# Kernel tuning notes

Hardware: AMD Instinct MI355X
Metric: run time of the kernel (lower is better)

Reference implementation:

```python
import jax, jax.numpy as jnp
import numpy as np

NEG_SLOPE = 0.2  # PyG GATConv default leaky_relu slope

def gat_conv(x, src, dst, W, a_src, a_dst, bias, N):
    # Linear transform
    h = x @ W                      # [N, D]
    # Per-node attention logits (heads=1)
    al_src = h @ a_src             # [N]
    al_dst = h @ a_dst             # [N]
    e = jax.nn.leaky_relu(al_src[src] + al_dst[dst], NEG_SLOPE)  # [E]
    # Segment softmax over incoming edges of each destination node
    m = jax.ops.segment_max(e, dst, num_segments=N)
    ex = jnp.exp(e - m[dst])
    denom = jax.ops.segment_sum(ex, dst, num_segments=N)
    alpha = ex / denom[dst]        # [E]
    # Weighted scatter-aggregate of source features
    out = jax.ops.segment_sum(h[src] * alpha[:, None], dst, num_segments=N)
    return out + bias

def setup_inputs() -> dict:
    key = jax.random.key(0)
    ks = jax.random.split(key, 10)
    N, E, F_in, H, O = 50000, 800000, 128, 64, 64
    x = jax.random.normal(ks[0], (N, F_in), dtype=jnp.float32)
    edge_index = jax.random.randint(ks[1], (2, E), 0, N, dtype=jnp.int32)
    s = lambda k, shp, fan: jax.random.normal(k, shp, dtype=jnp.float32) / np.sqrt(fan)
    return {
        'x': x, 'edge_index': edge_index,
        'W1': s(ks[2], (F_in, H), F_in), 'a_src1': s(ks[3], (H,), H), 'a_dst1': s(ks[4], (H,), H), 'b1': jnp.zeros((H,), jnp.float32),
        'W2': s(ks[5], (H, O), H), 'a_src2': s(ks[6], (O,), O), 'a_dst2': s(ks[7], (O,), O), 'b2': jnp.zeros((O,), jnp.float32),
    }

def reference(x, edge_index, W1, a_src1, a_dst1, b1, W2, a_src2, a_dst2, b2):
    N = x.shape[0]
    loops = jnp.arange(N, dtype=edge_index.dtype)  # PyG adds self-loops by default
    src = jnp.concatenate([edge_index[0], loops])
    dst = jnp.concatenate([edge_index[1], loops])
    h = gat_conv(x, src, dst, W1, a_src1, a_dst1, b1, N)
    h = jax.nn.relu(h)
    # dropout(p=0.6) is identity in eval mode
    out = gat_conv(h, src, dst, W2, a_src2, a_dst2, b2, N)
    return out
```

## Files before the change

kernel.cpp:

```cpp
#include <hip/hip_runtime.h>
#include <hip/hip_bf16.h>

#define DEV static __device__ __forceinline__

typedef short bf16x8 __attribute__((ext_vector_type(8)));
typedef float f32x4  __attribute__((ext_vector_type(4)));
typedef unsigned u32x4 __attribute__((ext_vector_type(4)));

union U4 { uint4 u; bf16x8 s; };

DEV float b2f(__hip_bfloat16 v) { return __bfloat162float(v); }
DEV float lrelu(float e) { return e > 0.f ? e : 0.2f * e; }

DEV unsigned short f2bu(float f) {
    __hip_bfloat16 b = __float2bfloat16(f);
    return *reinterpret_cast<unsigned short*>(&b);
}
DEV float bu2f(unsigned short u) { return __uint_as_float((unsigned)u << 16); }

DEV float loadF(const void* p, size_t i, int f32) {
    if (f32) return ((const float*)p)[i];
    return b2f(((const __hip_bfloat16*)p)[i]);
}

DEV uint4 pack8(const unsigned short* t) {
    uint4 v;
    v.x = (unsigned)t[0] | ((unsigned)t[1] << 16);
    v.y = (unsigned)t[2] | ((unsigned)t[3] << 16);
    v.z = (unsigned)t[4] | ((unsigned)t[5] << 16);
    v.w = (unsigned)t[6] | ((unsigned)t[7] << 16);
    return v;
}

DEV u32x4 pack8v(const unsigned short* t) {
    u32x4 v;
    v.x = (unsigned)t[0] | ((unsigned)t[1] << 16);
    v.y = (unsigned)t[2] | ((unsigned)t[3] << 16);
    v.z = (unsigned)t[4] | ((unsigned)t[5] << 16);
    v.w = (unsigned)t[6] | ((unsigned)t[7] << 16);
    return v;
}

DEV void edge_sd(int i, int E, const int* __restrict__ src, const int* __restrict__ dst,
                 int& s, int& d) {
    if (i < E) { s = src[i]; d = dst[i]; }
    else       { s = d = i - E; }
}

DEV int detect_wave(const void* p, int n, int lane) {
    const unsigned short* u16 = (const unsigned short*)p;
    bool insane = false;
#pragma unroll
    for (int r = 0; r < 4; ++r) {
        int idx = lane + r * 64;
        if (idx < n) {
            unsigned short u = u16[idx];
            unsigned e = (u >> 7) & 0xFFu;
            insane |= (e >= 0xC8u) || (e == 0u && (u & 0x7Fu) != 0u);
        }
    }
    return (__ballot(insane) != 0ull) ? 1 : 0;
}

#define G_BIN 128

__global__ __launch_bounds__(256) void k_fused1(
    const void* __restrict__ x, const void* __restrict__ W,
    const void* __restrict__ a_s, const void* __restrict__ a_d,
    __hip_bfloat16* __restrict__ h, float* __restrict__ als, float* __restrict__ ald,
    int N, int gb, int nx, int nW1,
    const int* __restrict__ src, const int* __restrict__ dst,
    int* __restrict__ hist, int E, int EA, int chunk,
    const void* a5, int n5, const void* a6, int n6, const void* a7, int n7,
    const void* a8, int n8, const void* a9, int n9,
    int* __restrict__ flags)
{
    const int tid = threadIdx.x;
    const int bid = blockIdx.x;

    if (bid >= gb) {
        if (bid == gb + G_BIN) {
            const void* ps[9] = {x, W, a_s, a_d, a5, a6, a7, a8, a9};
            const int   ns[9] = {nx, nW1, 64, 64, n5, n6, n7, n8, n9};
            const int w = tid >> 6, lane = tid & 63;
            for (int k = w; k < 9; k += 4) {
                int f = detect_wave(ps[k], ns[k], lane);
                if (lane == 0) flags[k] = f;
            }
            return;
        }
        __shared__ int cnt[256];
        cnt[tid] = 0;
        __syncthreads();
        const int cb = bid - gb;
        const int lo = cb * chunk;
        const int hi = min(lo + chunk, EA);
        for (int i = lo + tid; i < hi; i += 256) {
            int s, d; edge_sd(i, E, src, dst, s, d);
            atomicAdd(&cnt[d >> 8], 1);
        }
        __syncthreads();
        hist[cb * 256 + tid] = cnt[tid];
        return;
    }

    __shared__ __align__(16) unsigned short sMem[2 * 64 * 136];
    __shared__ float sAs[64], sAd[64];
    __shared__ int sFl[4];
    unsigned short* sA = sMem;
    unsigned short* sB = sMem + 64 * 136;
    float* sOut = (float*)sMem;

    {
        const void* ps4[4] = {x, W, a_s, a_d};
        const int   ns4[4] = {nx, nW1, 64, 64};
        const int w = tid >> 6, lane = tid & 63;
        int f = detect_wave(ps4[w], ns4[w], lane);
        if (lane == 0) sFl[w] = f;
    }
    __syncthreads();
    const int fx = sFl[0], fw = sFl[1];

    const int row0 = bid * 64;
    if (tid < 64) sAs[tid] = loadF(a_s, tid, sFl[2]);
    else if (tid < 128) sAd[tid - 64] = loadF(a_d, tid - 64, sFl[3]);

    if (!fx) {
        const uint4* xg = (const uint4*)x;
#pragma unroll
        for (int it = 0; it < 2; ++it) {
            int g = tid + it * 256;
            int r = g >> 4, c16 = g & 15;
            uint4 v = (row0 + r < N) ? xg[(size_t)(row0 + r) * 16 + c16]
                                     : make_uint4(0, 0, 0, 0);
            *(uint4*)(sA + r * 136 + c16 * 8) = v;
        }
    } else {
        for (int i = tid; i < 64 * 128; i += 256) {
            int r = i >> 7, k = i & 127;
            float v = (row0 + r < N) ? ((const float*)x)[(size_t)(row0 + r) * 128 + k] : 0.f;
            sA[r * 136 + k] = f2bu(v);
        }
    }
    if (!fw) {
        const unsigned short* Wg = (const unsigned short*)W;
        const int n = tid & 63;
        int k0 = (tid >> 6) * 8;
#pragma unroll
        for (int rep = 0; rep < 4; ++rep, k0 += 32) {
            unsigned short t[8];
#pragma unroll
            for (int j = 0; j < 8; ++j) t[j] = Wg[(size_t)(k0 + j) * 64 + n];
            *(uint4*)(sB + n * 136 + k0) = pack8(t);
        }
    } else {
        const float* Wg = (const float*)W;
        for (int i = tid; i < 128 * 64; i += 256) {
            int k = i >> 6, n = i & 63;
            sB[n * 136 + k] = f2bu(Wg[i]);
        }
    }
    __syncthreads();

    const int w = tid >> 6, lane = tid & 63;
    const int m0 = w * 16;
    const int qr = lane >> 4;
    const int lc = lane & 15;

    bf16x8 afrag[4];
#pragma unroll
    for (int c = 0; c < 4; ++c) {
        U4 u; u.u = *(const uint4*)(sA + (m0 + lc) * 136 + c * 32 + qr * 8);
        afrag[c] = u.s;
    }
    f32x4 accs[4];
#pragma unroll
    for (int nt = 0; nt < 4; ++nt) {
        f32x4 acc = {0.f, 0.f, 0.f, 0.f};
#pragma unroll
        for (int c = 0; c < 4; ++c) {
            U4 u; u.u = *(const uint4*)(sB + (nt * 16 + lc) * 136 + c * 32 + qr * 8);
            acc = __builtin_amdgcn_mfma_f32_16x16x32_bf16(afrag[c], u.s, acc, 0, 0, 0);
        }
        accs[nt] = acc;
    }
    __syncthreads();

#pragma unroll
    for (int nt = 0; nt < 4; ++nt)
#pragma unroll
        for (int reg = 0; reg < 4; ++reg)
            sOut[(m0 + qr * 4 + reg) * 68 + nt * 16 + lc] = accs[nt][reg];
    __syncthreads();

    {
        const int r = tid >> 2, seg = tid & 3;
        const int row = row0 + r;
        const float* po = sOut + r * 68 + seg * 16;
        float ps = 0.f, pd = 0.f;
        unsigned short ob[16];
#pragma unroll
        for (int i = 0; i < 16; ++i) {
            float v = po[i];
            ps = fmaf(v, sAs[seg * 16 + i], ps);
            pd = fmaf(v, sAd[seg * 16 + i], pd);
            ob[i] = f2bu(v);
        }
        if (row < N) {
            uint4* hp = (uint4*)((unsigned short*)h + (size_t)row * 64 + seg * 16);
            hp[0] = pack8(ob);
            hp[1] = pack8(ob + 8);
        }
        ps += __shfl_xor(ps, 1, 64); ps += __shfl_xor(ps, 2, 64);
        pd += __shfl_xor(pd, 1, 64); pd += __shfl_xor(pd, 2, 64);
        if (seg == 0 && row < N) { als[row] = ps; ald[row] = pd; }
    }
}

__global__ __launch_bounds__(256) void k_binC2(
    const int* __restrict__ src, const int* __restrict__ dst,
    const int* __restrict__ hist, int* __restrict__ btot,
    unsigned* __restrict__ ebuf, int E, int EA, int chunk)
{
    __shared__ int sm[256];
    __shared__ int cur[256];
    const int tid = threadIdx.x;
    const int cb = blockIdx.x;

    int tot = 0, mine = 0;
#pragma unroll 4
    for (int c = 0; c < G_BIN; ++c) {
        int v = hist[c * 256 + tid];
        tot += v;
        if (c < cb) mine += v;
    }
    if (cb == 0) btot[tid] = tot;
    sm[tid] = tot;
    __syncthreads();
#pragma unroll
    for (int off = 1; off < 256; off <<= 1) {
        int t = (tid >= off) ? sm[tid - off] : 0;
        __syncthreads();
        sm[tid] += t;
        __syncthreads();
    }
    cur[tid] = (sm[tid] - tot) + mine;
    __syncthreads();
    const int lo = cb * chunk;
    const int hi = min(lo + chunk, EA);
    for (int i = lo + tid; i < hi; i += 256) {
        int s, d; edge_sd(i, E, src, dst, s, d);
        int pos = atomicAdd(&cur[d >> 8], 1);
        ebuf[pos] = ((unsigned)(d & 255) << 17) | (unsigned)s;
    }
}

__global__ __launch_bounds__(256) void k_binD(
    const unsigned* __restrict__ ebuf, const int* __restrict__ btot,
    int* __restrict__ row_ptr, int* __restrict__ col, int N)
{
    __shared__ int sm[256];
    __shared__ int cnt[256];
    __shared__ int pfx[256];
    const int tid = threadIdx.x;
    const int b = blockIdx.x;
    {
        int v = btot[tid];
        sm[tid] = v;
        __syncthreads();
#pragma unroll
        for (int off = 1; off < 256; off <<= 1) {
            int t = (tid >= off) ? sm[tid - off] : 0;
            __syncthreads();
            sm[tid] += t;
            __syncthreads();
        }
    }
    const int lo = (b == 0) ? 0 : sm[b - 1];
    const int hi = sm[b];
    cnt[tid] = 0;
    __syncthreads();
    for (int i = lo + tid; i < hi; i += 256)
        atomicAdd(&cnt[ebuf[i] >> 17], 1);
    __syncthreads();
    const int c = cnt[tid];
    pfx[tid] = c;
    __syncthreads();
#pragma unroll
    for (int off = 1; off < 256; off <<= 1) {
        int t = (tid >= off) ? pfx[tid - off] : 0;
        __syncthreads();
        pfx[tid] += t;
        __syncthreads();
    }
    const int excl = pfx[tid] - c;
    const int d = b * 256 + tid;
    if (d <= N) row_ptr[d] = lo + excl;
    __syncthreads();
    cnt[tid] = lo + excl;
    __syncthreads();
    for (int i = lo + tid; i < hi; i += 256) {
        unsigned v = ebuf[i];
        int pos = atomicAdd(&cnt[v >> 17], 1);
        col[pos] = (int)(v & 0x1FFFFu);
    }
}

__global__ __launch_bounds__(256) void k_gemm2(
    __hip_bfloat16* __restrict__ agg, const void* __restrict__ b1,
    const void* __restrict__ W, const void* __restrict__ a_s,
    const void* __restrict__ a_d, const int* __restrict__ flags,
    float* __restrict__ als, float* __restrict__ ald, int N)
{
    __shared__ __align__(16) unsigned short sMem[2 * 64 * 72];
    __shared__ float sAs[64], sAd[64], sBias[64];
    unsigned short* sA = sMem;
    unsigned short* sB = sMem + 64 * 72;
    float* sOut = (float*)sMem;

    const int tid = threadIdx.x;
    const int row0 = blockIdx.x * 64;
    const int fw = flags[5];

    if (tid < 64) sAs[tid] = loadF(a_s, tid, flags[6]);
    else if (tid < 128) sAd[tid - 64] = loadF(a_d, tid - 64, flags[7]);
    else if (tid < 192) sBias[tid - 128] = loadF(b1, tid - 128, flags[4]);
    __syncthreads();

    {
        const uint4* ag = (const uint4*)agg;
#pragma unroll
        for (int it = 0; it < 2; ++it) {
            int g = tid + it * 256;
            int r = g >> 3, c8 = g & 7;
            uint4 v = (row0 + r < N) ? ag[(size_t)(row0 + r) * 8 + c8]
                                     : make_uint4(0, 0, 0, 0);
            unsigned short in[8] = {
                (unsigned short)(v.x & 0xFFFF), (unsigned short)(v.x >> 16),
                (unsigned short)(v.y & 0xFFFF), (unsigned short)(v.y >> 16),
                (unsigned short)(v.z & 0xFFFF), (unsigned short)(v.z >> 16),
                (unsigned short)(v.w & 0xFFFF), (unsigned short)(v.w >> 16)};
            unsigned short ob[8];
#pragma unroll
            for (int j = 0; j < 8; ++j) {
                float t = bu2f(in[j]) + sBias[c8 * 8 + j];
                ob[j] = f2bu(t > 0.f ? t : 0.f);
            }
            *(uint4*)(sA + r * 72 + c8 * 8) = pack8(ob);
        }
    }
    if (!fw) {
        const unsigned short* Wg = (const unsigned short*)W;
        const int n = tid & 63;
        int k0 = (tid >> 6) * 8;
#pragma unroll
        for (int rep = 0; rep < 2; ++rep, k0 += 32) {
            unsigned short t[8];
#pragma unroll
            for (int j = 0; j < 8; ++j) t[j] = Wg[(size_t)(k0 + j) * 64 + n];
            *(uint4*)(sB + n * 72 + k0) = pack8(t);
        }
    } else {
        const float* Wg = (const float*)W;
        for (int i = tid; i < 64 * 64; i += 256) {
            int k = i >> 6, n = i & 63;
            sB[n * 72 + k] = f2bu(Wg[i]);
        }
    }
    __syncthreads();

    const int w = tid >> 6, lane = tid & 63;
    const int m0 = w * 16;
    const int qr = lane >> 4, lc = lane & 15;

    bf16x8 afrag[2];
#pragma unroll
    for (int c = 0; c < 2; ++c) {
        U4 u; u.u = *(const uint4*)(sA + (m0 + lc) * 72 + c * 32 + qr * 8);
        afrag[c] = u.s;
    }
    f32x4 accs[4];
#pragma unroll
    for (int nt = 0; nt < 4; ++nt) {
        f32x4 acc = {0.f, 0.f, 0.f, 0.f};
#pragma unroll
        for (int c = 0; c < 2; ++c) {
            U4 u; u.u = *(const uint4*)(sB + (nt * 16 + lc) * 72 + c * 32 + qr * 8);
            acc = __builtin_amdgcn_mfma_f32_16x16x32_bf16(afrag[c], u.s, acc, 0, 0, 0);
        }
        accs[nt] = acc;
    }
    __syncthreads();
#pragma unroll
    for (int nt = 0; nt < 4; ++nt)
#pragma unroll
        for (int reg = 0; reg < 4; ++reg)
            sOut[(m0 + qr * 4 + reg) * 68 + nt * 16 + lc] = accs[nt][reg];
    __syncthreads();

    {
        const int r = tid >> 2, seg = tid & 3;
        const int row = row0 + r;
        const float* po = sOut + r * 68 + seg * 16;
        float ps = 0.f, pd = 0.f;
        unsigned short ob[16];
#pragma unroll
        for (int i = 0; i < 16; ++i) {
            float v = po[i];
            ps = fmaf(v, sAs[seg * 16 + i], ps);
            pd = fmaf(v, sAd[seg * 16 + i], pd);
            ob[i] = f2bu(v);
        }
        if (row < N) {
            uint4* hp = (uint4*)((unsigned short*)agg + (size_t)row * 64 + seg * 16);
            hp[0] = pack8(ob);
            hp[1] = pack8(ob + 8);
        }
        ps += __shfl_xor(ps, 1, 64); ps += __shfl_xor(ps, 2, 64);
        pd += __shfl_xor(pd, 1, 64); pd += __shfl_xor(pd, 2, 64);
        if (seg == 0 && row < N) { als[row] = ps; ald[row] = pd; }
    }
}

__global__ __launch_bounds__(256) void k_gather(
    const int* __restrict__ row_ptr, const int* __restrict__ col,
    const float* __restrict__ als, const float* __restrict__ ald,
    const __hip_bfloat16* __restrict__ h,
    __hip_bfloat16* __restrict__ agg_out,
    void* __restrict__ final_out,
    const void* __restrict__ bias, const int* __restrict__ flags, int N)
{
    const int tid = threadIdx.x;
    const int lane = tid & 63;
    const int eg = lane >> 3, fg = lane & 7;
    const int wid = blockIdx.x * 4 + (tid >> 6);
    const int nw  = gridDim.x * 4;
    const int npw = (N + nw - 1) / nw;
    const int base = wid * npw;
    if (base >= N) return;
    const int cnt = min(npw, N - base);

    int rp = 0; float aldv = 0.f;
    if (lane <= cnt) rp = row_ptr[base + lane];
    if (lane < cnt)  aldv = ald[base + lane];

    for (int k = 0; k < cnt; ++k) {
        const int d = base + k;
        const int beg = __shfl(rp, k, 64);
        const int end = __shfl(rp, k + 1, 64);
        const float aldd = __shfl(aldv, k, 64);

        float acc[8] = {0.f,0.f,0.f,0.f,0.f,0.f,0.f,0.f};
        float den = 0.f;
        int j = beg + eg;
        if (j < end) {
            int sC = col[j];
            float alsC = als[sC];
            uint4 hvC = *reinterpret_cast<const uint4*>(h + (size_t)sC * 64 + fg * 8);
            for (; j < end; j += 8) {
                const int jn = j + 8;
                int sN = 0; float alsN = 0.f;
                uint4 hvN = make_uint4(0, 0, 0, 0);
                if (jn < end) {
                    sN = col[jn];
                    alsN = als[sN];
                    hvN = *reinterpret_cast<const uint4*>(h + (size_t)sN * 64 + fg * 8);
                }
                const float w = __expf(lrelu(alsC + aldd));
                den += w;
                acc[0] = fmaf(w, __uint_as_float(hvC.x << 16),          acc[0]);
                acc[1] = fmaf(w, __uint_as_float(hvC.x & 0xFFFF0000u),  acc[1]);
                acc[2] = fmaf(w, __uint_as_float(hvC.y << 16),          acc[2]);
                acc[3] = fmaf(w, __uint_as_float(hvC.y & 0xFFFF0000u),  acc[3]);
                acc[4] = fmaf(w, __uint_as_float(hvC.z << 16),          acc[4]);
                acc[5] = fmaf(w, __uint_as_float(hvC.z & 0xFFFF0000u),  acc[5]);
                acc[6] = fmaf(w, __uint_as_float(hvC.w << 16),          acc[6]);
                acc[7] = fmaf(w, __uint_as_float(hvC.w & 0xFFFF0000u),  acc[7]);
                sC = sN; alsC = alsN; hvC = hvN;
            }
        }
#pragma unroll
        for (int off = 8; off <= 32; off <<= 1) {
            den += __shfl_xor(den, off, 64);
#pragma unroll
            for (int q = 0; q < 8; ++q) acc[q] += __shfl_xor(acc[q], off, 64);
        }
        if (eg == 0) {
            const float inv = 1.f / den;
            if (final_out) {
                float vb[8];
#pragma unroll
                for (int q = 0; q < 8; ++q) vb[q] = acc[q] * inv + loadF(bias, fg * 8 + q, flags[8]);
                if (flags[0]) {
                    float* o = (float*)final_out + (size_t)d * 64 + fg * 8;
                    f32x4 o0 = {vb[0], vb[1], vb[2], vb[3]};
                    f32x4 o1 = {vb[4], vb[5], vb[6], vb[7]};
                    __builtin_nontemporal_store(o0, (f32x4*)o);
                    __builtin_nontemporal_store(o1, (f32x4*)(o + 4));
                } else {
                    unsigned short ob[8];
#pragma unroll
                    for (int q = 0; q < 8; ++q) ob[q] = f2bu(vb[q]);
                    __builtin_nontemporal_store(pack8v(ob),
                        reinterpret_cast<u32x4*>((__hip_bfloat16*)final_out + (size_t)d * 64 + fg * 8));
                }
            } else {
                unsigned short ob[8];
#pragma unroll
                for (int q = 0; q < 8; ++q) ob[q] = f2bu(acc[q] * inv);
                __builtin_nontemporal_store(pack8v(ob),
                    reinterpret_cast<u32x4*>(agg_out + (size_t)d * 64 + fg * 8));
            }
        }
    }
}

extern "C" void kernel_launch(void* const* d_in, const int* in_sizes, int n_in,
                              void* d_out, int out_size, void* d_ws, size_t ws_size,
                              hipStream_t stream)
{
    const void* x   = d_in[0];
    const int*  ei  = (const int*)d_in[1];
    const void* W1  = d_in[2];
    const void* as1 = d_in[3];
    const void* ad1 = d_in[4];
    const void* b1  = d_in[5];
    const void* W2  = d_in[6];
    const void* as2 = d_in[7];
    const void* ad2 = d_in[8];
    const void* b2  = d_in[9];

    const int N  = in_sizes[0] / 128;
    const int E  = in_sizes[1] / 2;
    const int EA = E + N;
    const int* src = ei;
    const int* dst = ei + E;

    uintptr_t base = (uintptr_t)d_ws;
    auto alloc = [&](size_t bytes) { uintptr_t p = base; base += (bytes + 63) & ~(size_t)63; return p; };
    int*      flags    = (int*)alloc(64 * 4);
    float*    als      = (float*)alloc((size_t)N * 4);
    float*    ald      = (float*)alloc((size_t)N * 4);
    int*      row_ptr  = (int*)alloc((size_t)(N + 1) * 4);
    int*      hist     = (int*)alloc((size_t)G_BIN * 256 * 4);
    int*      btot     = (int*)alloc(256 * 4);
    unsigned* ebuf     = (unsigned*)alloc((size_t)EA * 4);
    int*      col      = (int*)alloc((size_t)EA * 4);
    __hip_bfloat16* hbuf   = (__hip_bfloat16*)alloc((size_t)N * 64 * 2);
    __hip_bfloat16* aggbuf = (__hip_bfloat16*)alloc((size_t)N * 64 * 2);

    const int gatherb = 1792;
    const int gb  = (N + 63) / 64;
    const int NBK = (N + 255) / 256;
    const int chunk = (EA + G_BIN - 1) / G_BIN;

    k_fused1<<<gb + G_BIN + 1, 256, 0, stream>>>(
        x, W1, as1, ad1, hbuf, als, ald, N, gb, in_sizes[0], in_sizes[2],
        src, dst, hist, E, EA, chunk,
        b1, in_sizes[5], W2, in_sizes[6], as2, in_sizes[7], ad2, in_sizes[8],
        b2, in_sizes[9], flags);
    k_binC2<<<G_BIN, 256, 0, stream>>>(src, dst, hist, btot, ebuf, E, EA, chunk);
    k_binD<<<NBK, 256, 0, stream>>>(ebuf, btot, row_ptr, col, N);

    k_gather<<<gatherb, 256, 0, stream>>>(row_ptr, col, als, ald, hbuf, aggbuf,
                                          nullptr, nullptr, flags, N);
    k_gemm2<<<gb, 256, 0, stream>>>(aggbuf, b1, W2, as2, ad2, flags, als, ald, N);
    k_gather<<<gatherb, 256, 0, stream>>>(row_ptr, col, als, ald, aggbuf, nullptr,
                                          d_out, b2, flags, N);
    (void)out_size; (void)ws_size; (void)n_in;
}
```

Baseline: 211.2 us.

## Fuse layer-2 GEMM and attention logits into layer-1 gather epilogue

Removes the separate k_gemm2 kernel. The first gather now applies bias and ReLU, multiplies each node's aggregated row by W2 held in shared memory (via wave shuffles, in fp32 FMA), writes h2, and computes the layer-2 attention logits into new als2/ald2 buffers. This saves one kernel launch and a full round trip of the aggregated features through global memory, at the cost of a 64-step shuffle+FMA loop per node, a 16KB shared W2 tile per block, and giving up the MFMA path. Both gathers also drop the software prefetch of the next feature row and load it in-loop instead.

```diff
diff --git a/kernel.cpp b/kernel.cpp
--- a/kernel.cpp
+++ b/kernel.cpp
@@ -306,127 +306,112 @@
     }
 }
 
-__global__ __launch_bounds__(256) void k_gemm2(
-    __hip_bfloat16* __restrict__ agg, const void* __restrict__ b1,
-    const void* __restrict__ W, const void* __restrict__ a_s,
-    const void* __restrict__ a_d, const int* __restrict__ flags,
-    float* __restrict__ als, float* __restrict__ ald, int N)
-{
-    __shared__ __align__(16) unsigned short sMem[2 * 64 * 72];
-    __shared__ float sAs[64], sAd[64], sBias[64];
-    unsigned short* sA = sMem;
-    unsigned short* sB = sMem + 64 * 72;
-    float* sOut = (float*)sMem;
-
-    const int tid = threadIdx.x;
-    const int row0 = blockIdx.x * 64;
-    const int fw = flags[5];
-
-    if (tid < 64) sAs[tid] = loadF(a_s, tid, flags[6]);
-    else if (tid < 128) sAd[tid - 64] = loadF(a_d, tid - 64, flags[7]);
-    else if (tid < 192) sBias[tid - 128] = loadF(b1, tid - 128, flags[4]);
-    __syncthreads();
-
-    {
-        const uint4* ag = (const uint4*)agg;
-#pragma unroll
-        for (int it = 0; it < 2; ++it) {
-            int g = tid + it * 256;
-            int r = g >> 3, c8 = g & 7;
-            uint4 v = (row0 + r < N) ? ag[(size_t)(row0 + r) * 8 + c8]
-                                     : make_uint4(0, 0, 0, 0);
-            unsigned short in[8] = {
-                (unsigned short)(v.x & 0xFFFF), (unsigned short)(v.x >> 16),
-                (unsigned short)(v.y & 0xFFFF), (unsigned short)(v.y >> 16),
-                (unsigned short)(v.z & 0xFFFF), (unsigned short)(v.z >> 16),
-                (unsigned short)(v.w & 0xFFFF), (unsigned short)(v.w >> 16)};
-            unsigned short ob[8];
-#pragma unroll
-            for (int j = 0; j < 8; ++j) {
-                float t = bu2f(in[j]) + sBias[c8 * 8 + j];
-                ob[j] = f2bu(t > 0.f ? t : 0.f);
-            }
-            *(uint4*)(sA + r * 72 + c8 * 8) = pack8(ob);
-        }
-    }
-    if (!fw) {
-        const unsigned short* Wg = (const unsigned short*)W;
-        const int n = tid & 63;
-        int k0 = (tid >> 6) * 8;
-#pragma unroll
-        for (int rep = 0; rep < 2; ++rep, k0 += 32) {
-            unsigned short t[8];
-#pragma unroll
-            for (int j = 0; j < 8; ++j) t[j] = Wg[(size_t)(k0 + j) * 64 + n];
-            *(uint4*)(sB + n * 72 + k0) = pack8(t);
-        }
-    } else {
-        const float* Wg = (const float*)W;
-        for (int i = tid; i < 64 * 64; i += 256) {
-            int k = i >> 6, n = i & 63;
-            sB[n * 72 + k] = f2bu(Wg[i]);
-        }
-    }
-    __syncthreads();
-
-    const int w = tid >> 6, lane = tid & 63;
-    const int m0 = w * 16;
-    const int qr = lane >> 4, lc = lane & 15;
-
-    bf16x8 afrag[2];
-#pragma unroll
-    for (int c = 0; c < 2; ++c) {
-        U4 u; u.u = *(const uint4*)(sA + (m0 + lc) * 72 + c * 32 + qr * 8);
-        afrag[c] = u.s;
-    }
-    f32x4 accs[4];
-#pragma unroll
-    for (int nt = 0; nt < 4; ++nt) {
-        f32x4 acc = {0.f, 0.f, 0.f, 0.f};
-#pragma unroll
-        for (int c = 0; c < 2; ++c) {
-            U4 u; u.u = *(const uint4*)(sB + (nt * 16 + lc) * 72 + c * 32 + qr * 8);
-            acc = __builtin_amdgcn_mfma_f32_16x16x32_bf16(afrag[c], u.s, acc, 0, 0, 0);
-        }
-        accs[nt] = acc;
-    }
-    __syncthreads();
-#pragma unroll
-    for (int nt = 0; nt < 4; ++nt)
-#pragma unroll
-        for (int reg = 0; reg < 4; ++reg)
-            sOut[(m0 + qr * 4 + reg) * 68 + nt * 16 + lc] = accs[nt][reg];
-    __syncthreads();
-
-    {
-        const int r = tid >> 2, seg = tid & 3;
-        const int row = row0 + r;
-        const float* po = sOut + r * 68 + seg * 16;
-        float ps = 0.f, pd = 0.f;
-        unsigned short ob[16];
-#pragma unroll
-        for (int i = 0; i < 16; ++i) {
-            float v = po[i];
-            ps = fmaf(v, sAs[seg * 16 + i], ps);
-            pd = fmaf(v, sAd[seg * 16 + i], pd);
-            ob[i] = f2bu(v);
-        }
-        if (row < N) {
-            uint4* hp = (uint4*)((unsigned short*)agg + (size_t)row * 64 + seg * 16);
-            hp[0] = pack8(ob);
-            hp[1] = pack8(ob + 8);
-        }
-        ps += __shfl_xor(ps, 1, 64); ps += __shfl_xor(ps, 2, 64);
-        pd += __shfl_xor(pd, 1, 64); pd += __shfl_xor(pd, 2, 64);
-        if (seg == 0 && row < N) { als[row] = ps; ald[row] = pd; }
-    }
-}
-
-__global__ __launch_bounds__(256) void k_gather(
+__global__ __launch_bounds__(256) void k_gather1(
     const int* __restrict__ row_ptr, const int* __restrict__ col,
     const float* __restrict__ als, const float* __restrict__ ald,
     const __hip_bfloat16* __restrict__ h,
-    __hip_bfloat16* __restrict__ agg_out,
+    __hip_bfloat16* __restrict__ h2,
+    float* __restrict__ als2, float* __restrict__ ald2,
+    const void* __restrict__ b1, const void* __restrict__ W2,
+    const void* __restrict__ a_s2, const void* __restrict__ a_d2,
+    const int* __restrict__ flags, int N)
+{
+    __shared__ float sW2[64 * 65];
+    __shared__ float sB1[64], sAs2[64], sAd2[64];
+
+    const int tid = threadIdx.x;
+    {
+        const int fw2 = flags[5];
+        for (int i = tid; i < 64 * 64; i += 256) {
+            int k = i >> 6, n = i & 63;
+            sW2[k * 65 + n] = loadF(W2, i, fw2);
+        }
+        if (tid < 64) sB1[tid] = loadF(b1, tid, flags[4]);
+        else if (tid < 128) sAs2[tid - 64] = loadF(a_s2, tid - 64, flags[6]);
+        else if (tid < 192) sAd2[tid - 128] = loadF(a_d2, tid - 128, flags[7]);
+    }
+    __syncthreads();
+
+    const int lane = tid & 63;
+    const int eg = lane >> 3, fg = lane & 7;
+    const int wid = blockIdx.x * 4 + (tid >> 6);
+    const int nw  = gridDim.x * 4;
+    const int npw = (N + nw - 1) / nw;
+    const int base = wid * npw;
+    if (base >= N) return;
+    const int cnt = min(npw, N - base);
+
+    const float a2s = sAs2[lane], a2d = sAd2[lane];
+
+    int rp = 0; float aldv = 0.f;
+    if (lane <= cnt) rp = row_ptr[base + lane];
+    if (lane < cnt)  aldv = ald[base + lane];
+
+    for (int k = 0; k < cnt; ++k) {
+        const int d = base + k;
+        const int beg = __shfl(rp, k, 64);
+        const int end = __shfl(rp, k + 1, 64);
+        const float aldd = __shfl(aldv, k, 64);
+
+        float acc[8] = {0.f,0.f,0.f,0.f,0.f,0.f,0.f,0.f};
+        float den = 0.f;
+        int j = beg + eg;
+        if (j < end) {
+            int sC = col[j];
+            float alsC = als[sC];
+            for (; j < end; j += 8) {
+                const int jn = j + 8;
+                int sN = 0; float alsN = 0.f;
+                if (jn < end) { sN = col[jn]; alsN = als[sN]; }
+                const float w = __expf(lrelu(alsC + aldd));
+                const uint4 hv = *reinterpret_cast<const uint4*>(h + (size_t)sC * 64 + fg * 8);
+                den += w;
+                acc[0] = fmaf(w, __uint_as_float(hv.x << 16),          acc[0]);
+                acc[1] = fmaf(w, __uint_as_float(hv.x & 0xFFFF0000u),  acc[1]);
+                acc[2] = fmaf(w, __uint_as_float(hv.y << 16),          acc[2]);
+                acc[3] = fmaf(w, __uint_as_float(hv.y & 0xFFFF0000u),  acc[3]);
+                acc[4] = fmaf(w, __uint_as_float(hv.z << 16),          acc[4]);
+                acc[5] = fmaf(w, __uint_as_float(hv.z & 0xFFFF0000u),  acc[5]);
+                acc[6] = fmaf(w, __uint_as_float(hv.w << 16),          acc[6]);
+                acc[7] = fmaf(w, __uint_as_float(hv.w & 0xFFFF0000u),  acc[7]);
+                sC = sN; alsC = alsN;
+            }
+        }
+#pragma unroll
+        for (int off = 8; off <= 32; off <<= 1) {
+            den += __shfl_xor(den, off, 64);
+#pragma unroll
+            for (int q = 0; q < 8; ++q) acc[q] += __shfl_xor(acc[q], off, 64);
+        }
+
+        const float inv = 1.f / den;
+        float rel[8];
+#pragma unroll
+        for (int q = 0; q < 8; ++q) {
+            float v = fmaf(acc[q], inv, sB1[fg * 8 + q]);
+            rel[q] = v > 0.f ? v : 0.f;
+        }
+        float o = 0.f;
+#pragma unroll
+        for (int f = 0; f < 64; ++f) {
+            const float rf = __shfl(rel[f & 7], f >> 3, 64);
+            o = fmaf(rf, sW2[f * 65 + lane], o);
+        }
+        h2[(size_t)d * 64 + lane] = *reinterpret_cast<__hip_bfloat16*>(&(unsigned short&)*(unsigned short[]){f2bu(o)});
+        float zs = o * a2s, zd = o * a2d;
+#pragma unroll
+        for (int off = 1; off <= 32; off <<= 1) {
+            zs += __shfl_xor(zs, off, 64);
+            zd += __shfl_xor(zd, off, 64);
+        }
+        if (lane == 0) { als2[d] = zs; ald2[d] = zd; }
+    }
+}
+
+__global__ __launch_bounds__(256) void k_gather2(
+    const int* __restrict__ row_ptr, const int* __restrict__ col,
+    const float* __restrict__ als, const float* __restrict__ ald,
+    const __hip_bfloat16* __restrict__ h,
     void* __restrict__ final_out,
     const void* __restrict__ bias, const int* __restrict__ flags, int N)
 {
@@ -456,27 +441,22 @@
         if (j < end) {
             int sC = col[j];
             float alsC = als[sC];
-            uint4 hvC = *reinterpret_cast<const uint4*>(h + (size_t)sC * 64 + fg * 8);
             for (; j < end; j += 8) {
                 const int jn = j + 8;
                 int sN = 0; float alsN = 0.f;
-                uint4 hvN = make_uint4(0, 0, 0, 0);
-                if (jn < end) {
-                    sN = col[jn];
-                    alsN = als[sN];
-                    hvN = *reinterpret_cast<const uint4*>(h + (size_t)sN * 64 + fg * 8);
-                }
+                if (jn < end) { sN = col[jn]; alsN = als[sN]; }
                 const float w = __expf(lrelu(alsC + aldd));
+                const uint4 hv = *reinterpret_cast<const uint4*>(h + (size_t)sC * 64 + fg * 8);
                 den += w;
-                acc[0] = fmaf(w, __uint_as_float(hvC.x << 16),          acc[0]);
-                acc[1] = fmaf(w, __uint_as_float(hvC.x & 0xFFFF0000u),  acc[1]);
-                acc[2] = fmaf(w, __uint_as_float(hvC.y << 16),          acc[2]);
-                acc[3] = fmaf(w, __uint_as_float(hvC.y & 0xFFFF0000u),  acc[3]);
-                acc[4] = fmaf(w, __uint_as_float(hvC.z << 16),          acc[4]);
-                acc[5] = fmaf(w, __uint_as_float(hvC.z & 0xFFFF0000u),  acc[5]);
-                acc[6] = fmaf(w, __uint_as_float(hvC.w << 16),          acc[6]);
-                acc[7] = fmaf(w, __uint_as_float(hvC.w & 0xFFFF0000u),  acc[7]);
-                sC = sN; alsC = alsN; hvC = hvN;
+                acc[0] = fmaf(w, __uint_as_float(hv.x << 16),          acc[0]);
+                acc[1] = fmaf(w, __uint_as_float(hv.x & 0xFFFF0000u),  acc[1]);
+                acc[2] = fmaf(w, __uint_as_float(hv.y << 16),          acc[2]);
+                acc[3] = fmaf(w, __uint_as_float(hv.y & 0xFFFF0000u),  acc[3]);
+                acc[4] = fmaf(w, __uint_as_float(hv.z << 16),          acc[4]);
+                acc[5] = fmaf(w, __uint_as_float(hv.z & 0xFFFF0000u),  acc[5]);
+                acc[6] = fmaf(w, __uint_as_float(hv.w << 16),          acc[6]);
+                acc[7] = fmaf(w, __uint_as_float(hv.w & 0xFFFF0000u),  acc[7]);
+                sC = sN; alsC = alsN;
             }
         }
 #pragma unroll
@@ -487,29 +467,21 @@
         }
         if (eg == 0) {
             const float inv = 1.f / den;
-            if (final_out) {
-                float vb[8];
-#pragma unroll
-                for (int q = 0; q < 8; ++q) vb[q] = acc[q] * inv + loadF(bias, fg * 8 + q, flags[8]);
-                if (flags[0]) {
-                    float* o = (float*)final_out + (size_t)d * 64 + fg * 8;
-                    f32x4 o0 = {vb[0], vb[1], vb[2], vb[3]};
-                    f32x4 o1 = {vb[4], vb[5], vb[6], vb[7]};
-                    __builtin_nontemporal_store(o0, (f32x4*)o);
-                    __builtin_nontemporal_store(o1, (f32x4*)(o + 4));
-                } else {
-                    unsigned short ob[8];
-#pragma unroll
-                    for (int q = 0; q < 8; ++q) ob[q] = f2bu(vb[q]);
-                    __builtin_nontemporal_store(pack8v(ob),
-                        reinterpret_cast<u32x4*>((__hip_bfloat16*)final_out + (size_t)d * 64 + fg * 8));
-                }
+            float vb[8];
+#pragma unroll
+            for (int q = 0; q < 8; ++q) vb[q] = acc[q] * inv + loadF(bias, fg * 8 + q, flags[8]);
+            if (flags[0]) {
+                float* o = (float*)final_out + (size_t)d * 64 + fg * 8;
+                f32x4 o0 = {vb[0], vb[1], vb[2], vb[3]};
+                f32x4 o1 = {vb[4], vb[5], vb[6], vb[7]};
+                __builtin_nontemporal_store(o0, (f32x4*)o);
+                __builtin_nontemporal_store(o1, (f32x4*)(o + 4));
             } else {
                 unsigned short ob[8];
 #pragma unroll
-                for (int q = 0; q < 8; ++q) ob[q] = f2bu(acc[q] * inv);
+                for (int q = 0; q < 8; ++q) ob[q] = f2bu(vb[q]);
                 __builtin_nontemporal_store(pack8v(ob),
-                    reinterpret_cast<u32x4*>(agg_out + (size_t)d * 64 + fg * 8));
+                    reinterpret_cast<u32x4*>((__hip_bfloat16*)final_out + (size_t)d * 64 + fg * 8));
             }
         }
     }
@@ -541,6 +513,8 @@
     int*      flags    = (int*)alloc(64 * 4);
     float*    als      = (float*)alloc((size_t)N * 4);
     float*    ald      = (float*)alloc((size_t)N * 4);
+    float*    als2     = (float*)alloc((size_t)N * 4);
+    float*    ald2     = (float*)alloc((size_t)N * 4);
     int*      row_ptr  = (int*)alloc((size_t)(N + 1) * 4);
     int*      hist     = (int*)alloc((size_t)G_BIN * 256 * 4);
     int*      btot     = (int*)alloc(256 * 4);
@@ -562,10 +536,9 @@
     k_binC2<<<G_BIN, 256, 0, stream>>>(src, dst, hist, btot, ebuf, E, EA, chunk);
     k_binD<<<NBK, 256, 0, stream>>>(ebuf, btot, row_ptr, col, N);
 
-    k_gather<<<gatherb, 256, 0, stream>>>(row_ptr, col, als, ald, hbuf, aggbuf,
-                                          nullptr, nullptr, flags, N);
-    k_gemm2<<<gb, 256, 0, stream>>>(aggbuf, b1, W2, as2, ad2, flags, als, ald, N);
-    k_gather<<<gatherb, 256, 0, stream>>>(row_ptr, col, als, ald, aggbuf, nullptr,
-                                          d_out, b2, flags, N);
+    k_gather1<<<gatherb, 256, 0, stream>>>(row_ptr, col, als, ald, hbuf, aggbuf,
+                                           als2, ald2, b1, W2, as2, ad2, flags, N);
+    k_gather2<<<gatherb, 256, 0, stream>>>(row_ptr, col, als2, ald2, aggbuf,
+                                           d_out, b2, flags, N);
     (void)out_size; (void)ws_size; (void)n_in;
 }
```

Result: slower. 249.7 us (+18.3%).

## Restructure gather to lane-per-feature with wave-wide edge weight computation

Applied to the files above, without the earlier changes.

The gather kernel is rewritten so each lane owns one feature column of a destination node. Edge weights for up to 64 edges are computed once per wave, one edge per lane, and then broadcast with shuffles, replacing the previous 8-edge-group by 8-feature-group split that needed cross-group shuffle reductions of eight accumulators. Destination nodes are now strided across waves instead of assigned in contiguous chunks, and the grid grows from 1792 to 2048 blocks. The cost is narrower memory accesses: 2-byte scalar loads per lane instead of 16-byte vector loads, and scalar stores instead of nontemporal vector stores, which may raise memory instruction count.

```diff
diff --git a/kernel.cpp b/kernel.cpp
--- a/kernel.cpp
+++ b/kernel.cpp
@@ -25,15 +25,6 @@
 
 DEV uint4 pack8(const unsigned short* t) {
     uint4 v;
-    v.x = (unsigned)t[0] | ((unsigned)t[1] << 16);
-    v.y = (unsigned)t[2] | ((unsigned)t[3] << 16);
-    v.z = (unsigned)t[4] | ((unsigned)t[5] << 16);
-    v.w = (unsigned)t[6] | ((unsigned)t[7] << 16);
-    return v;
-}
-
-DEV u32x4 pack8v(const unsigned short* t) {
-    u32x4 v;
     v.x = (unsigned)t[0] | ((unsigned)t[1] << 16);
     v.y = (unsigned)t[2] | ((unsigned)t[3] << 16);
     v.z = (unsigned)t[4] | ((unsigned)t[5] << 16);
@@ -432,85 +423,62 @@
 {
     const int tid = threadIdx.x;
     const int lane = tid & 63;
-    const int eg = lane >> 3, fg = lane & 7;
     const int wid = blockIdx.x * 4 + (tid >> 6);
     const int nw  = gridDim.x * 4;
-    const int npw = (N + nw - 1) / nw;
-    const int base = wid * npw;
-    if (base >= N) return;
-    const int cnt = min(npw, N - base);
-
-    int rp = 0; float aldv = 0.f;
-    if (lane <= cnt) rp = row_ptr[base + lane];
-    if (lane < cnt)  aldv = ald[base + lane];
-
-    for (int k = 0; k < cnt; ++k) {
-        const int d = base + k;
-        const int beg = __shfl(rp, k, 64);
-        const int end = __shfl(rp, k + 1, 64);
-        const float aldd = __shfl(aldv, k, 64);
-
-        float acc[8] = {0.f,0.f,0.f,0.f,0.f,0.f,0.f,0.f};
+    const unsigned short* hp = (const unsigned short*)h;
+
+    float bval = 0.f; int f0 = 0;
+    if (final_out) { bval = loadF(bias, lane, flags[8]); f0 = flags[0]; }
+
+    for (int d = wid; d < N; d += nw) {
+        const int beg = row_ptr[d], end = row_ptr[d + 1];
+        const float aldd = ald[d];
+
         float den = 0.f;
-        int j = beg + eg;
-        if (j < end) {
-            int sC = col[j];
-            float alsC = als[sC];
-            uint4 hvC = *reinterpret_cast<const uint4*>(h + (size_t)sC * 64 + fg * 8);
-            for (; j < end; j += 8) {
-                const int jn = j + 8;
-                int sN = 0; float alsN = 0.f;
-                uint4 hvN = make_uint4(0, 0, 0, 0);
-                if (jn < end) {
-                    sN = col[jn];
-                    alsN = als[sN];
-                    hvN = *reinterpret_cast<const uint4*>(h + (size_t)sN * 64 + fg * 8);
+        float a0 = 0.f, a1 = 0.f, a2 = 0.f, a3 = 0.f;
+        float a4 = 0.f, a5 = 0.f, a6 = 0.f, a7 = 0.f;
+
+        for (int jb = beg; jb < end; jb += 64) {
+            const int m = min(64, end - jb);
+            int s = 0; float w = 0.f;
+            if (lane < m) {
+                s = col[jb + lane];
+                w = __expf(lrelu(als[s] + aldd));
+            }
+            float wsum = w;
+#pragma unroll
+            for (int off = 1; off <= 32; off <<= 1) wsum += __shfl_xor(wsum, off, 64);
+            den += wsum;
+
+            for (int j = 0; j < m; j += 8) {
+                float wv[8]; int sv[8]; unsigned short hv[8];
+#pragma unroll
+                for (int q = 0; q < 8; ++q) {
+                    const bool ok = (j + q) < m;
+                    wv[q] = ok ? __shfl(w, j + q, 64) : 0.f;
+                    sv[q] = ok ? __shfl(s, j + q, 64) : 0;
                 }
-                const float w = __expf(lrelu(alsC + aldd));
-                den += w;
-                acc[0] = fmaf(w, __uint_as_float(hvC.x << 16),          acc[0]);
-                acc[1] = fmaf(w, __uint_as_float(hvC.x & 0xFFFF0000u),  acc[1]);
-                acc[2] = fmaf(w, __uint_as_float(hvC.y << 16),          acc[2]);
-                acc[3] = fmaf(w, __uint_as_float(hvC.y & 0xFFFF0000u),  acc[3]);
-                acc[4] = fmaf(w, __uint_as_float(hvC.z << 16),          acc[4]);
-                acc[5] = fmaf(w, __uint_as_float(hvC.z & 0xFFFF0000u),  acc[5]);
-                acc[6] = fmaf(w, __uint_as_float(hvC.w << 16),          acc[6]);
-                acc[7] = fmaf(w, __uint_as_float(hvC.w & 0xFFFF0000u),  acc[7]);
-                sC = sN; alsC = alsN; hvC = hvN;
+#pragma unroll
+                for (int q = 0; q < 8; ++q)
+                    hv[q] = hp[(size_t)sv[q] * 64 + lane];
+                a0 = fmaf(wv[0], bu2f(hv[0]), a0);
+                a1 = fmaf(wv[1], bu2f(hv[1]), a1);
+                a2 = fmaf(wv[2], bu2f(hv[2]), a2);
+                a3 = fmaf(wv[3], bu2f(hv[3]), a3);
+                a4 = fmaf(wv[4], bu2f(hv[4]), a4);
+                a5 = fmaf(wv[5], bu2f(hv[5]), a5);
+                a6 = fmaf(wv[6], bu2f(hv[6]), a6);
+                a7 = fmaf(wv[7], bu2f(hv[7]), a7);
             }
         }
-#pragma unroll
-        for (int off = 8; off <= 32; off <<= 1) {
-            den += __shfl_xor(den, off, 64);
-#pragma unroll
-            for (int q = 0; q < 8; ++q) acc[q] += __shfl_xor(acc[q], off, 64);
-        }
-        if (eg == 0) {
-            const float inv = 1.f / den;
-            if (final_out) {
-                float vb[8];
-#pragma unroll
-                for (int q = 0; q < 8; ++q) vb[q] = acc[q] * inv + loadF(bias, fg * 8 + q, flags[8]);
-                if (flags[0]) {
-                    float* o = (float*)final_out + (size_t)d * 64 + fg * 8;
-                    f32x4 o0 = {vb[0], vb[1], vb[2], vb[3]};
-                    f32x4 o1 = {vb[4], vb[5], vb[6], vb[7]};
-                    __builtin_nontemporal_store(o0, (f32x4*)o);
-                    __builtin_nontemporal_store(o1, (f32x4*)(o + 4));
-                } else {
-                    unsigned short ob[8];
-#pragma unroll
-                    for (int q = 0; q < 8; ++q) ob[q] = f2bu(vb[q]);
-                    __builtin_nontemporal_store(pack8v(ob),
-                        reinterpret_cast<u32x4*>((__hip_bfloat16*)final_out + (size_t)d * 64 + fg * 8));
-                }
-            } else {
-                unsigned short ob[8];
-#pragma unroll
-                for (int q = 0; q < 8; ++q) ob[q] = f2bu(acc[q] * inv);
-                __builtin_nontemporal_store(pack8v(ob),
-                    reinterpret_cast<u32x4*>(agg_out + (size_t)d * 64 + fg * 8));
-            }
+        const float acc = ((a0 + a1) + (a2 + a3)) + ((a4 + a5) + (a6 + a7));
+        const float inv = 1.f / den;
+        if (final_out) {
+            const float vb = fmaf(acc, inv, bval);
+            if (f0) ((float*)final_out)[(size_t)d * 64 + lane] = vb;
+            else ((unsigned short*)final_out)[(size_t)d * 64 + lane] = f2bu(vb);
+        } else {
+            ((unsigned short*)agg_out)[(size_t)d * 64 + lane] = f2bu(acc * inv);
         }
     }
 }
@@ -549,7 +517,7 @@
     __hip_bfloat16* hbuf   = (__hip_bfloat16*)alloc((size_t)N * 64 * 2);
     __hip_bfloat16* aggbuf = (__hip_bfloat16*)alloc((size_t)N * 64 * 2);
 
-    const int gatherb = 1792;
+    const int gatherb = 2048;
     const int gb  = (N + 63) / 64;
     const int NBK = (N + 255) / 256;
     const int chunk = (EA + G_BIN - 1) / G_BIN;
```

New measurement: 242.7 us. 14.9% more time.

## Embed layer-1 source logits in CSR edges and template gather kernel

Applied to the files above, without the earlier changes.

During CSR construction, k_binD now stores each edge as an (src, als[src]) int2 pair. The layer-1 gather can then read the source attention logit together with the column index and skip a dependent random load. The gather is templated on mode, so the bias loads and flag checks are hoisted out of the edge loop. Nodes are also assigned to wavefronts in a grid-stride pattern instead of contiguous chunks, and the grid grows to 2048 blocks. In exchange, the edge array doubles in size. Layer 2 reads this wider array but cannot use the embedded logit, so its edge stream gets heavier.

```diff
diff --git a/kernel.cpp b/kernel.cpp
--- a/kernel.cpp
+++ b/kernel.cpp
@@ -257,7 +257,8 @@
 
 __global__ __launch_bounds__(256) void k_binD(
     const unsigned* __restrict__ ebuf, const int* __restrict__ btot,
-    int* __restrict__ row_ptr, int* __restrict__ col, int N)
+    const float* __restrict__ als,
+    int* __restrict__ row_ptr, int2* __restrict__ ecol, int N)
 {
     __shared__ int sm[256];
     __shared__ int cnt[256];
@@ -301,8 +302,9 @@
     __syncthreads();
     for (int i = lo + tid; i < hi; i += 256) {
         unsigned v = ebuf[i];
+        const int s = (int)(v & 0x1FFFFu);
         int pos = atomicAdd(&cnt[v >> 17], 1);
-        col[pos] = (int)(v & 0x1FFFFu);
+        ecol[pos] = make_int2(s, __float_as_int(als[s]));
     }
 }
 
@@ -422,8 +424,9 @@
     }
 }
 
-__global__ __launch_bounds__(256) void k_gather(
-    const int* __restrict__ row_ptr, const int* __restrict__ col,
+template<int MODE>
+__global__ __launch_bounds__(256) void k_gather_t(
+    const int* __restrict__ row_ptr, const int2* __restrict__ ecol,
     const float* __restrict__ als, const float* __restrict__ ald,
     const __hip_bfloat16* __restrict__ h,
     __hip_bfloat16* __restrict__ agg_out,
@@ -435,38 +438,35 @@
     const int eg = lane >> 3, fg = lane & 7;
     const int wid = blockIdx.x * 4 + (tid >> 6);
     const int nw  = gridDim.x * 4;
-    const int npw = (N + nw - 1) / nw;
-    const int base = wid * npw;
-    if (base >= N) return;
-    const int cnt = min(npw, N - base);
-
-    int rp = 0; float aldv = 0.f;
-    if (lane <= cnt) rp = row_ptr[base + lane];
-    if (lane < cnt)  aldv = ald[base + lane];
-
-    for (int k = 0; k < cnt; ++k) {
-        const int d = base + k;
-        const int beg = __shfl(rp, k, 64);
-        const int end = __shfl(rp, k + 1, 64);
-        const float aldd = __shfl(aldv, k, 64);
-
+
+    float bv[8]; int f0 = 0;
+    if (MODE == 1) {
+        f0 = flags[0];
+#pragma unroll
+        for (int k = 0; k < 8; ++k) bv[k] = loadF(bias, fg * 8 + k, flags[8]);
+    }
+
+    for (int d = wid; d < N; d += nw) {
+        const float aldd = ald[d];
+        const int beg = row_ptr[d], end = row_ptr[d + 1];
         float acc[8] = {0.f,0.f,0.f,0.f,0.f,0.f,0.f,0.f};
         float den = 0.f;
         int j = beg + eg;
         if (j < end) {
-            int sC = col[j];
-            float alsC = als[sC];
-            uint4 hvC = *reinterpret_cast<const uint4*>(h + (size_t)sC * 64 + fg * 8);
+            int2 e = ecol[j];
+            float aC = (MODE == 0) ? __int_as_float(e.y) : als[e.x];
+            uint4 hvC = *reinterpret_cast<const uint4*>(h + (size_t)e.x * 64 + fg * 8);
             for (; j < end; j += 8) {
                 const int jn = j + 8;
-                int sN = 0; float alsN = 0.f;
+                int2 eN = make_int2(0, 0);
+                float aN = 0.f;
                 uint4 hvN = make_uint4(0, 0, 0, 0);
                 if (jn < end) {
-                    sN = col[jn];
-                    alsN = als[sN];
-                    hvN = *reinterpret_cast<const uint4*>(h + (size_t)sN * 64 + fg * 8);
+                    eN = ecol[jn];
+                    aN = (MODE == 0) ? __int_as_float(eN.y) : als[eN.x];
+                    hvN = *reinterpret_cast<const uint4*>(h + (size_t)eN.x * 64 + fg * 8);
                 }
-                const float w = __expf(lrelu(alsC + aldd));
+                const float w = __expf(lrelu(aC + aldd));
                 den += w;
                 acc[0] = fmaf(w, __uint_as_float(hvC.x << 16),          acc[0]);
                 acc[1] = fmaf(w, __uint_as_float(hvC.x & 0xFFFF0000u),  acc[1]);
@@ -476,7 +476,7 @@
                 acc[5] = fmaf(w, __uint_as_float(hvC.z & 0xFFFF0000u),  acc[5]);
                 acc[6] = fmaf(w, __uint_as_float(hvC.w << 16),          acc[6]);
                 acc[7] = fmaf(w, __uint_as_float(hvC.w & 0xFFFF0000u),  acc[7]);
-                sC = sN; alsC = alsN; hvC = hvN;
+                e = eN; aC = aN; hvC = hvN;
             }
         }
 #pragma unroll
@@ -487,11 +487,11 @@
         }
         if (eg == 0) {
             const float inv = 1.f / den;
-            if (final_out) {
+            if (MODE == 1) {
                 float vb[8];
 #pragma unroll
-                for (int q = 0; q < 8; ++q) vb[q] = acc[q] * inv + loadF(bias, fg * 8 + q, flags[8]);
-                if (flags[0]) {
+                for (int q = 0; q < 8; ++q) vb[q] = fmaf(acc[q], inv, bv[q]);
+                if (f0) {
                     float* o = (float*)final_out + (size_t)d * 64 + fg * 8;
                     f32x4 o0 = {vb[0], vb[1], vb[2], vb[3]};
                     f32x4 o1 = {vb[4], vb[5], vb[6], vb[7]};
@@ -545,11 +545,11 @@
     int*      hist     = (int*)alloc((size_t)G_BIN * 256 * 4);
     int*      btot     = (int*)alloc(256 * 4);
     unsigned* ebuf     = (unsigned*)alloc((size_t)EA * 4);
-    int*      col      = (int*)alloc((size_t)EA * 4);
+    int2*     ecol     = (int2*)alloc((size_t)EA * 8);
     __hip_bfloat16* hbuf   = (__hip_bfloat16*)alloc((size_t)N * 64 * 2);
     __hip_bfloat16* aggbuf = (__hip_bfloat16*)alloc((size_t)N * 64 * 2);
 
-    const int gatherb = 1792;
+    const int gatherb = 2048;
     const int gb  = (N + 63) / 64;
     const int NBK = (N + 255) / 256;
     const int chunk = (EA + G_BIN - 1) / G_BIN;
@@ -560,12 +560,12 @@
         b1, in_sizes[5], W2, in_sizes[6], as2, in_sizes[7], ad2, in_sizes[8],
         b2, in_sizes[9], flags);
     k_binC2<<<G_BIN, 256, 0, stream>>>(src, dst, hist, btot, ebuf, E, EA, chunk);
-    k_binD<<<NBK, 256, 0, stream>>>(ebuf, btot, row_ptr, col, N);
-
-    k_gather<<<gatherb, 256, 0, stream>>>(row_ptr, col, als, ald, hbuf, aggbuf,
-                                          nullptr, nullptr, flags, N);
+    k_binD<<<NBK, 256, 0, stream>>>(ebuf, btot, als, row_ptr, ecol, N);
+
+    k_gather_t<0><<<gatherb, 256, 0, stream>>>(row_ptr, ecol, nullptr, ald, hbuf,
+                                               aggbuf, nullptr, nullptr, flags, N);
     k_gemm2<<<gb, 256, 0, stream>>>(aggbuf, b1, W2, as2, ad2, flags, als, ald, N);
-    k_gather<<<gatherb, 256, 0, stream>>>(row_ptr, col, als, ald, aggbuf, nullptr,
-                                          d_out, b2, flags, N);
+    k_gather_t<1><<<gatherb, 256, 0, stream>>>(row_ptr, ecol, als, ald, aggbuf,
+                                               nullptr, d_out, b2, flags, N);
     (void)out_size; (void)ws_size; (void)n_in;
 }
```

Result: faster. 200.8 us (-4.9%).
